# Kernel optimization log

Measured on AMD Instinct MI355X. Metric: run time of the kernel, lower is better.

The kernel has to match this reference:

```python
import jax, jax.numpy as jnp
import numpy as np

N_ANGLES = 180
N_DETECTORS = 256


def _bilinear_sample(img, x, y):
    """Bilinear sample img[y, x]; zero outside. img: [H, W]; x, y: any shape."""
    H, W = img.shape
    x0 = jnp.floor(x)
    y0 = jnp.floor(y)
    xi = x0.astype(jnp.int32)
    yi = y0.astype(jnp.int32)
    wx = x - x0
    wy = y - y0

    def get(ix, iy):
        valid = (ix >= 0) & (ix < W) & (iy >= 0) & (iy < H)
        ixc = jnp.clip(ix, 0, W - 1)
        iyc = jnp.clip(iy, 0, H - 1)
        return jnp.where(valid, img[iyc, ixc], jnp.zeros((), img.dtype))

    v00 = get(xi, yi)
    v01 = get(xi + 1, yi)
    v10 = get(xi, yi + 1)
    v11 = get(xi + 1, yi + 1)
    return (v00 * (1.0 - wx) + v01 * wx) * (1.0 - wy) + (v10 * (1.0 - wx) + v11 * wx) * wy


def setup_inputs() -> dict:
    key = jax.random.key(0)
    inputs = jax.random.uniform(key, (8, 256, 256, 1), dtype=jnp.float32)
    return {"inputs": inputs}


def reference(inputs):
    # Parallel-beam forward Radon transform (forwardproject).
    # inputs: [B, H, W, 1] image batch -> sinogram [B, n_angles, n_detectors, 1]
    B, H, W, _ = inputs.shape
    A, D = N_ANGLES, N_DETECTORS
    T = H  # integration samples along each ray

    theta = jnp.linspace(0.0, jnp.pi, A, endpoint=False, dtype=inputs.dtype)
    cos_t = jnp.cos(theta)[:, None, None]  # [A,1,1]
    sin_t = jnp.sin(theta)[:, None, None]

    s = (jnp.arange(D, dtype=inputs.dtype) - (D - 1) / 2.0)[None, :, None]  # detector offsets
    t = (jnp.arange(T, dtype=inputs.dtype) - (T - 1) / 2.0)[None, None, :]  # along-ray offsets

    cx = (W - 1) / 2.0
    cy = (H - 1) / 2.0
    # sample coords for every (angle, detector, ray-step): [A, D, T]
    x = cx + s * cos_t - t * sin_t
    y = cy + s * sin_t + t * cos_t

    imgs = inputs[..., 0]  # [B, H, W]
    vals = jax.vmap(lambda im: _bilinear_sample(im, x, y))(imgs)  # [B, A, D, T]
    sino = vals.sum(axis=-1)  # ray integral (unit step length)
    return sino[..., None]  # [B, A, D, 1]
```

## Files before the change

### kernel.cpp

```cpp
#include <hip/hip_runtime.h>
#include <math.h>

#define NA    180
#define HB    9
#define KB    29
#define PC    262
#define PR    263
#define TROWS 11
#define TSZ   (PC * TROWS)
#define OUTN  (8 * NA * 256)
#define APG   4
#define NG    23

typedef _Float16 h2  __attribute__((ext_vector_type(2)));
typedef _Float16 h8  __attribute__((ext_vector_type(8)));
typedef __fp16   hf2 __attribute__((ext_vector_type(2)));

__device__ __forceinline__ h2 pkrtz(float a, float b) {
    hf2 t = __builtin_amdgcn_cvt_pkrtz(a, b);
    return __builtin_bit_cast(h2, t);
}
__device__ __forceinline__ float fdot2f(h2 a, h2 b, float c) {
#if __has_builtin(__builtin_amdgcn_fdot2)
    return __builtin_amdgcn_fdot2(__builtin_bit_cast(hf2, a),
                                  __builtin_bit_cast(hf2, b), c, false);
#else
    return c + (float)a.x * (float)b.x + (float)a.y * (float)b.y;
#endif
}
__device__ __forceinline__ float imc(const float* im, int y, int x) {
    return ((unsigned)y < 256u && (unsigned)x < 256u) ? im[(y << 8) + x] : 0.0f;
}

__global__ __launch_bounds__(256) void prep_kernel(
    const float* __restrict__ img, uint4* __restrict__ P0,
    uint4* __restrict__ P1, float* __restrict__ out, float* __restrict__ tab)
{
    const int tid = threadIdx.x;
    const int row = blockIdx.x;
    const int mb  = blockIdx.y;

    if (mb == 0) {
        for (int i = row * 256 + tid; i < OUTN; i += PR * 256) out[i] = 0.0f;
    }
    if (mb == 1 && row == 0 && tid < NA) {
        const float theta = (float)tid * ((float)M_PI / (float)NA);
        tab[tid]      = cosf(theta);
        tab[tid + NA] = sinf(theta);
    }

    const int bg = mb & 1;
    const float* im0 = img + ((size_t)(bg * 4) << 16);
    const int v = row - 3;

    if (mb < 2) {
        uint4* dst = P0 + (size_t)(bg * PR + row) * PC;
        for (int j = tid; j < PC; j += 256) {
            const int u = j - 2;
            h8 t = {};
            if (j < 261) {
                t[0] = (_Float16)imc(im0,             v, u); t[1] = (_Float16)imc(im0,             v + 1, u);
                t[2] = (_Float16)imc(im0 + (1 << 16), v, u); t[3] = (_Float16)imc(im0 + (1 << 16), v + 1, u);
                t[4] = (_Float16)imc(im0 + (2 << 16), v, u); t[5] = (_Float16)imc(im0 + (2 << 16), v + 1, u);
                t[6] = (_Float16)imc(im0 + (3 << 16), v, u); t[7] = (_Float16)imc(im0 + (3 << 16), v + 1, u);
            }
            dst[j] = __builtin_bit_cast(uint4, t);
        }
    } else {
        uint4* dst = P1 + (size_t)(bg * PR + row) * PC;
        for (int j = tid; j < PC; j += 256) {
            const int u = j - 2;
            h8 t = {};
            if (j < 261) {
                t[0] = (_Float16)imc(im0,             u, v); t[1] = (_Float16)imc(im0,             u, v + 1);
                t[2] = (_Float16)imc(im0 + (1 << 16), u, v); t[3] = (_Float16)imc(im0 + (1 << 16), u, v + 1);
                t[4] = (_Float16)imc(im0 + (2 << 16), u, v); t[5] = (_Float16)imc(im0 + (2 << 16), u, v + 1);
                t[6] = (_Float16)imc(im0 + (3 << 16), u, v); t[7] = (_Float16)imc(im0 + (3 << 16), u, v + 1);
            }
            dst[j] = __builtin_bit_cast(uint4, t);
        }
    }
}

#define SAMPLE(JV, UV, VPV, A0, A1, A2, A3)                                   \
    {                                                                         \
        const float ucl = fminf(fmaxf((UV), -1.5f), 257.5f);                  \
        const float uf = floorf(ucl);                                         \
        const float wu = ucl - uf;                                            \
        const float vf = floorf(VPV);                                         \
        const float wv = (VPV) - vf;                                          \
        const float vfc = fminf(fmaxf(vf, -1.0f), 9.0f);                      \
        const int idx = (int)fmaf(vfc, (float)PC, uf) + (PC + 2);             \
        const h8 A8 = __builtin_bit_cast(h8, s_tile[idx]);                    \
        const h8 B8 = __builtin_bit_cast(h8, s_tile[idx + 1]);                \
        const h2 wu2 = pkrtz(wu, wu);                                         \
        const h8 wu8 = __builtin_shufflevector(wu2, wu2, 0,1,0,1,0,1,0,1);    \
        const h8 tb8 = (B8 - A8) * wu8 + A8;                                  \
        h2 wv2 = pkrtz(1.0f - wv, wv);                                        \
        wv2 = ((unsigned)(JV) < span) ? wv2 : hz;                             \
        A0 = fdot2f(__builtin_shufflevector(tb8, tb8, 0, 1), wv2, A0);        \
        A1 = fdot2f(__builtin_shufflevector(tb8, tb8, 2, 3), wv2, A1);        \
        A2 = fdot2f(__builtin_shufflevector(tb8, tb8, 4, 5), wv2, A2);        \
        A3 = fdot2f(__builtin_shufflevector(tb8, tb8, 6, 7), wv2, A3);        \
    }

template<bool MODEX>
__device__ __forceinline__ void radon_body(
    const uint4* __restrict__ Pbase,
    float* __restrict__ out, const float* __restrict__ tab,
    uint4* s_tile, int tid, int b0, int p, int gi)
{
    const int lo = -2 + p * HB;

    {
        const uint4* src = Pbase + (size_t)(lo + 2) * PC;
        for (int i = tid; i < TSZ; i += 256) s_tile[i] = src[i];
    }
    __syncthreads();

    const float detf = (float)tid - 127.5f;
    const float lof = (float)lo;
    const h2 hz = {};

    for (int g = 0; g < APG; ++g) {
        const int ai = gi * APG + g;
        int a;
        if (MODEX) { if (ai >= 89) break; a = 46 + ai; }
        else       { if (ai >= 91) break; a = (ai <= 45) ? ai : 89 + ai; }

        const float c = tab[a];
        const float s = tab[a + NA];

        const float xc = 127.5f + detf * c + 127.5f * s;
        const float yc = 127.5f + detf * s - 127.5f * c;

        const float ucst = MODEX ? yc : xc;
        const float vcst = MODEX ? xc : yc;
        const float du   = MODEX ? c  : -s;
        const float dv   = MODEX ? -s : c;

        const float inv = 1.0f / dv;
        const float f1 = (lof - vcst) * inv;
        const float f2 = (lof + (float)HB - vcst) * inv;
        const float fmn = fminf(f1, f2);
        const float fmx = fmaxf(f1, f2);
        int kmin, kend;
        if (dv > 0.0f) { kmin = (int)ceilf(fmn);      kend = (int)ceilf(fmx); }
        else           { kmin = (int)floorf(fmn) + 1; kend = (int)floorf(fmx) + 1; }

        const int len = kend - kmin;
        const int jlo = max(0, -kmin);
        const int jhi = min(len, 256 - kmin);
        const int spani = max(0, jhi - jlo);
        if (!__any(spani > 0)) continue;
        const unsigned span = (unsigned)spani;

        const int kstart = kmin + jlo;
        const int Lmax = (int)((float)HB * fabsf(inv)) + 2;

        float u  = fmaf((float)kstart, du, ucst);
        float vp = fmaf((float)kstart, dv, vcst - lof);
        const float du2 = du + du, dv2 = dv + dv;
        const float du3 = du2 + du, dv3 = dv2 + dv;
        const float du4 = du2 + du2, dv4 = dv2 + dv2;

        float a0 = 0.f, a1 = 0.f, a2 = 0.f, a3 = 0.f;
        float e0 = 0.f, e1 = 0.f, e2 = 0.f, e3 = 0.f;
        float c0 = 0.f, c1 = 0.f, c2 = 0.f, c3 = 0.f;
        float d0 = 0.f, d1 = 0.f, d2 = 0.f, d3 = 0.f;

        int j = 0;
        for (; j + 3 < Lmax; j += 4) {
            SAMPLE(j,     u,        vp,        a0, a1, a2, a3);
            SAMPLE(j + 1, u + du,   vp + dv,   e0, e1, e2, e3);
            SAMPLE(j + 2, u + du2,  vp + dv2,  c0, c1, c2, c3);
            SAMPLE(j + 3, u + du3,  vp + dv3,  d0, d1, d2, d3);
            u += du4; vp += dv4;
        }
        for (; j + 1 < Lmax; j += 2) {
            SAMPLE(j,     u,      vp,      a0, a1, a2, a3);
            SAMPLE(j + 1, u + du, vp + dv, e0, e1, e2, e3);
            u += du2; vp += dv2;
        }
        if (j < Lmax) SAMPLE(j, u, vp, a0, a1, a2, a3);

        if (spani > 0) {
            float* o = &out[((b0 * NA + a) << 8) + tid];
            atomicAdd(o,                 (a0 + c0) + (e0 + d0));
            atomicAdd(o + (NA << 8),     (a1 + c1) + (e1 + d1));
            atomicAdd(o + 2 * (NA << 8), (a2 + c2) + (e2 + d2));
            atomicAdd(o + 3 * (NA << 8), (a3 + c3) + (e3 + d3));
        }
    }
}

__global__ __launch_bounds__(256, 3) void radon_kernel(
    const uint4* __restrict__ P0, const uint4* __restrict__ P1,
    float* __restrict__ out, const float* __restrict__ tab)
{
    __shared__ uint4 s_tile[TSZ];
    const int tid = threadIdx.x;
    const int bg  = blockIdx.x;
    const int p   = blockIdx.y;
    const int gid = blockIdx.z;
    const int b0  = bg * 4;
    if (gid < NG)
        radon_body<false>(P0 + (size_t)bg * PR * PC, out, tab, s_tile, tid, b0, p, gid);
    else
        radon_body<true>(P1 + (size_t)bg * PR * PC, out, tab, s_tile, tid, b0, p, gid - NG);
}

extern "C" void kernel_launch(void* const* d_in, const int* in_sizes, int n_in,
                              void* d_out, int out_size, void* d_ws, size_t ws_size,
                              hipStream_t stream) {
    const float* img = (const float*)d_in[0];
    float* out = (float*)d_out;

    uint4* P0 = (uint4*)d_ws;
    uint4* P1 = P0 + (size_t)2 * PR * PC;
    float* tab = (float*)(P1 + (size_t)2 * PR * PC);

    prep_kernel<<<dim3(PR, 4), 256, 0, stream>>>(img, P0, P1, out, tab);
    radon_kernel<<<dim3(2, KB, 2 * NG), 256, 0, stream>>>(P0, P1, out, tab);
}
```

Before: 112.2 us.

## Pack all 8 batch images per texel and bilinear-sample in fp32 accumulators

The prep kernel now packs all 8 batch images into one 16-byte texel per pixel, where before it packed 4 images times 2 rows. Each sample therefore does 4 LDS reads and serves all 8 batches, and interpolation along v is done in fp16 with the u weight folded into fp32 FMAs instead of fdot2. Tiles are 8 rows tall, there are 2 angles per group, occupancy rises to 4 blocks, and the per-angle loop length becomes a wave-max span computed with shuffles instead of a fixed Lmax. The intent is to cut redundant index math and sample bookkeeping across batch groups. In exchange each sample issues more LDS loads and more FMAs per lane, and the accumulators use more registers.

New measurement: 108.5 us. -3.3%, faster.

```diff
diff --git a/kernel.cpp b/kernel.cpp
--- a/kernel.cpp
+++ b/kernel.cpp
@@ -2,15 +2,16 @@
 #include <math.h>
 
 #define NA    180
-#define HB    9
-#define KB    29
+#define HB    8
+#define KB    33
 #define PC    262
-#define PR    263
-#define TROWS 11
+#define PR    266
+#define TROWS 9
 #define TSZ   (PC * TROWS)
 #define OUTN  (8 * NA * 256)
-#define APG   4
-#define NG    23
+#define APG   2
+#define NGY   46
+#define NGX   45
 
 typedef _Float16 h2  __attribute__((ext_vector_type(2)));
 typedef _Float16 h8  __attribute__((ext_vector_type(8)));
@@ -19,14 +20,6 @@
 __device__ __forceinline__ h2 pkrtz(float a, float b) {
     hf2 t = __builtin_amdgcn_cvt_pkrtz(a, b);
     return __builtin_bit_cast(h2, t);
-}
-__device__ __forceinline__ float fdot2f(h2 a, h2 b, float c) {
-#if __has_builtin(__builtin_amdgcn_fdot2)
-    return __builtin_amdgcn_fdot2(__builtin_bit_cast(hf2, a),
-                                  __builtin_bit_cast(hf2, b), c, false);
-#else
-    return c + (float)a.x * (float)b.x + (float)a.y * (float)b.y;
-#endif
 }
 __device__ __forceinline__ float imc(const float* im, int y, int x) {
     return ((unsigned)y < 256u && (unsigned)x < 256u) ? im[(y << 8) + x] : 0.0f;
@@ -49,78 +42,80 @@
         tab[tid + NA] = sinf(theta);
     }
 
-    const int bg = mb & 1;
-    const float* im0 = img + ((size_t)(bg * 4) << 16);
     const int v = row - 3;
-
-    if (mb < 2) {
-        uint4* dst = P0 + (size_t)(bg * PR + row) * PC;
-        for (int j = tid; j < PC; j += 256) {
-            const int u = j - 2;
-            h8 t = {};
-            if (j < 261) {
-                t[0] = (_Float16)imc(im0,             v, u); t[1] = (_Float16)imc(im0,             v + 1, u);
-                t[2] = (_Float16)imc(im0 + (1 << 16), v, u); t[3] = (_Float16)imc(im0 + (1 << 16), v + 1, u);
-                t[4] = (_Float16)imc(im0 + (2 << 16), v, u); t[5] = (_Float16)imc(im0 + (2 << 16), v + 1, u);
-                t[6] = (_Float16)imc(im0 + (3 << 16), v, u); t[7] = (_Float16)imc(im0 + (3 << 16), v + 1, u);
+    uint4* dst = (mb == 0 ? P0 : P1) + (size_t)row * PC;
+    for (int j = tid; j < PC; j += 256) {
+        const int u = j - 2;
+        h8 t = {};
+        if (j < 261) {
+            if (mb == 0) {
+                #pragma unroll
+                for (int b = 0; b < 8; ++b)
+                    t[b] = (_Float16)imc(img + ((size_t)b << 16), v, u);
+            } else {
+                #pragma unroll
+                for (int b = 0; b < 8; ++b)
+                    t[b] = (_Float16)imc(img + ((size_t)b << 16), u, v);
             }
-            dst[j] = __builtin_bit_cast(uint4, t);
-        }
-    } else {
-        uint4* dst = P1 + (size_t)(bg * PR + row) * PC;
-        for (int j = tid; j < PC; j += 256) {
-            const int u = j - 2;
-            h8 t = {};
-            if (j < 261) {
-                t[0] = (_Float16)imc(im0,             u, v); t[1] = (_Float16)imc(im0,             u, v + 1);
-                t[2] = (_Float16)imc(im0 + (1 << 16), u, v); t[3] = (_Float16)imc(im0 + (1 << 16), u, v + 1);
-                t[4] = (_Float16)imc(im0 + (2 << 16), u, v); t[5] = (_Float16)imc(im0 + (2 << 16), u, v + 1);
-                t[6] = (_Float16)imc(im0 + (3 << 16), u, v); t[7] = (_Float16)imc(im0 + (3 << 16), u, v + 1);
-            }
-            dst[j] = __builtin_bit_cast(uint4, t);
-        }
-    }
-}
-
-#define SAMPLE(JV, UV, VPV, A0, A1, A2, A3)                                   \
+        }
+        dst[j] = __builtin_bit_cast(uint4, t);
+    }
+}
+
+#define SAMPLE8(JV, UV, VPV, ACC)                                             \
     {                                                                         \
         const float ucl = fminf(fmaxf((UV), -1.5f), 257.5f);                  \
         const float uf = floorf(ucl);                                         \
         const float wu = ucl - uf;                                            \
-        const float vf = floorf(VPV);                                         \
+        float vf = floorf(VPV);                                               \
+        vf = fminf(fmaxf(vf, 0.0f), 7.0f);                                    \
         const float wv = (VPV) - vf;                                          \
-        const float vfc = fminf(fmaxf(vf, -1.0f), 9.0f);                      \
-        const int idx = (int)fmaf(vfc, (float)PC, uf) + (PC + 2);             \
-        const h8 A8 = __builtin_bit_cast(h8, s_tile[idx]);                    \
-        const h8 B8 = __builtin_bit_cast(h8, s_tile[idx + 1]);                \
-        const h2 wu2 = pkrtz(wu, wu);                                         \
-        const h8 wu8 = __builtin_shufflevector(wu2, wu2, 0,1,0,1,0,1,0,1);    \
-        const h8 tb8 = (B8 - A8) * wu8 + A8;                                  \
-        h2 wv2 = pkrtz(1.0f - wv, wv);                                        \
-        wv2 = ((unsigned)(JV) < span) ? wv2 : hz;                             \
-        A0 = fdot2f(__builtin_shufflevector(tb8, tb8, 0, 1), wv2, A0);        \
-        A1 = fdot2f(__builtin_shufflevector(tb8, tb8, 2, 3), wv2, A1);        \
-        A2 = fdot2f(__builtin_shufflevector(tb8, tb8, 4, 5), wv2, A2);        \
-        A3 = fdot2f(__builtin_shufflevector(tb8, tb8, 6, 7), wv2, A3);        \
+        const int idx = (int)fmaf(vf, (float)PC, uf) + 2;                     \
+        const h8 ra0 = __builtin_bit_cast(h8, s_tile[idx]);                   \
+        const h8 ra1 = __builtin_bit_cast(h8, s_tile[idx + 1]);               \
+        const h8 rb0 = __builtin_bit_cast(h8, s_tile[idx + PC]);              \
+        const h8 rb1 = __builtin_bit_cast(h8, s_tile[idx + PC + 1]);          \
+        const h2 wv2 = pkrtz(wv, wv);                                         \
+        const h8 wv8 = __builtin_shufflevector(wv2, wv2, 0,1,0,1,0,1,0,1);    \
+        const h8 v0 = (rb0 - ra0) * wv8 + ra0;                                \
+        const h8 v1 = (rb1 - ra1) * wv8 + ra1;                                \
+        const float ws = ((unsigned)(JV) < span) ? 1.0f : 0.0f;               \
+        const float fw1 = ws * wu;                                            \
+        const float fw0 = ws - fw1;                                           \
+        ACC[0] = fmaf((float)v0[0], fw0, ACC[0]);                             \
+        ACC[0] = fmaf((float)v1[0], fw1, ACC[0]);                             \
+        ACC[1] = fmaf((float)v0[1], fw0, ACC[1]);                             \
+        ACC[1] = fmaf((float)v1[1], fw1, ACC[1]);                             \
+        ACC[2] = fmaf((float)v0[2], fw0, ACC[2]);                             \
+        ACC[2] = fmaf((float)v1[2], fw1, ACC[2]);                             \
+        ACC[3] = fmaf((float)v0[3], fw0, ACC[3]);                             \
+        ACC[3] = fmaf((float)v1[3], fw1, ACC[3]);                             \
+        ACC[4] = fmaf((float)v0[4], fw0, ACC[4]);                             \
+        ACC[4] = fmaf((float)v1[4], fw1, ACC[4]);                             \
+        ACC[5] = fmaf((float)v0[5], fw0, ACC[5]);                             \
+        ACC[5] = fmaf((float)v1[5], fw1, ACC[5]);                             \
+        ACC[6] = fmaf((float)v0[6], fw0, ACC[6]);                             \
+        ACC[6] = fmaf((float)v1[6], fw1, ACC[6]);                             \
+        ACC[7] = fmaf((float)v0[7], fw0, ACC[7]);                             \
+        ACC[7] = fmaf((float)v1[7], fw1, ACC[7]);                             \
     }
 
 template<bool MODEX>
 __device__ __forceinline__ void radon_body(
     const uint4* __restrict__ Pbase,
     float* __restrict__ out, const float* __restrict__ tab,
-    uint4* s_tile, int tid, int b0, int p, int gi)
+    uint4* s_tile, int tid, int p, int gi)
 {
     const int lo = -2 + p * HB;
 
     {
-        const uint4* src = Pbase + (size_t)(lo + 2) * PC;
+        const uint4* src = Pbase + (size_t)(lo + 3) * PC;
         for (int i = tid; i < TSZ; i += 256) s_tile[i] = src[i];
     }
     __syncthreads();
 
     const float detf = (float)tid - 127.5f;
     const float lof = (float)lo;
-    const h2 hz = {};
 
     for (int g = 0; g < APG; ++g) {
         const int ai = gi * APG + g;
@@ -139,9 +134,11 @@
         const float du   = MODEX ? c  : -s;
         const float dv   = MODEX ? -s : c;
 
+        const float vlo_f = fmaxf(lof, -1.0f);
+        const float vhi_f = fminf(lof + (float)HB, 256.0f);
         const float inv = 1.0f / dv;
-        const float f1 = (lof - vcst) * inv;
-        const float f2 = (lof + (float)HB - vcst) * inv;
+        const float f1 = (vlo_f - vcst) * inv;
+        const float f2 = (vhi_f - vcst) * inv;
         const float fmn = fminf(f1, f2);
         const float fmx = fmaxf(f1, f2);
         int kmin, kend;
@@ -152,11 +149,19 @@
         const int jlo = max(0, -kmin);
         const int jhi = min(len, 256 - kmin);
         const int spani = max(0, jhi - jlo);
-        if (!__any(spani > 0)) continue;
+
+        int m = spani;
+        m = max(m, __shfl_xor(m, 1));
+        m = max(m, __shfl_xor(m, 2));
+        m = max(m, __shfl_xor(m, 4));
+        m = max(m, __shfl_xor(m, 8));
+        m = max(m, __shfl_xor(m, 16));
+        m = max(m, __shfl_xor(m, 32));
+        const int mspan = __builtin_amdgcn_readfirstlane(m);
+        if (mspan <= 0) continue;
         const unsigned span = (unsigned)spani;
 
         const int kstart = kmin + jlo;
-        const int Lmax = (int)((float)HB * fabsf(inv)) + 2;
 
         float u  = fmaf((float)kstart, du, ucst);
         float vp = fmaf((float)kstart, dv, vcst - lof);
@@ -164,50 +169,45 @@
         const float du3 = du2 + du, dv3 = dv2 + dv;
         const float du4 = du2 + du2, dv4 = dv2 + dv2;
 
-        float a0 = 0.f, a1 = 0.f, a2 = 0.f, a3 = 0.f;
-        float e0 = 0.f, e1 = 0.f, e2 = 0.f, e3 = 0.f;
-        float c0 = 0.f, c1 = 0.f, c2 = 0.f, c3 = 0.f;
-        float d0 = 0.f, d1 = 0.f, d2 = 0.f, d3 = 0.f;
+        float accA[8] = {}, accB[8] = {}, accC[8] = {}, accD[8] = {};
 
         int j = 0;
-        for (; j + 3 < Lmax; j += 4) {
-            SAMPLE(j,     u,        vp,        a0, a1, a2, a3);
-            SAMPLE(j + 1, u + du,   vp + dv,   e0, e1, e2, e3);
-            SAMPLE(j + 2, u + du2,  vp + dv2,  c0, c1, c2, c3);
-            SAMPLE(j + 3, u + du3,  vp + dv3,  d0, d1, d2, d3);
+        for (; j + 3 < mspan; j += 4) {
+            SAMPLE8(j,     u,       vp,       accA);
+            SAMPLE8(j + 1, u + du,  vp + dv,  accB);
+            SAMPLE8(j + 2, u + du2, vp + dv2, accC);
+            SAMPLE8(j + 3, u + du3, vp + dv3, accD);
             u += du4; vp += dv4;
         }
-        for (; j + 1 < Lmax; j += 2) {
-            SAMPLE(j,     u,      vp,      a0, a1, a2, a3);
-            SAMPLE(j + 1, u + du, vp + dv, e0, e1, e2, e3);
+        for (; j + 1 < mspan; j += 2) {
+            SAMPLE8(j,     u,      vp,      accA);
+            SAMPLE8(j + 1, u + du, vp + dv, accB);
             u += du2; vp += dv2;
         }
-        if (j < Lmax) SAMPLE(j, u, vp, a0, a1, a2, a3);
+        if (j < mspan) SAMPLE8(j, u, vp, accA);
 
         if (spani > 0) {
-            float* o = &out[((b0 * NA + a) << 8) + tid];
-            atomicAdd(o,                 (a0 + c0) + (e0 + d0));
-            atomicAdd(o + (NA << 8),     (a1 + c1) + (e1 + d1));
-            atomicAdd(o + 2 * (NA << 8), (a2 + c2) + (e2 + d2));
-            atomicAdd(o + 3 * (NA << 8), (a3 + c3) + (e3 + d3));
-        }
-    }
-}
-
-__global__ __launch_bounds__(256, 3) void radon_kernel(
+            float* o = &out[(a << 8) + tid];
+            #pragma unroll
+            for (int b = 0; b < 8; ++b)
+                atomicAdd(o + b * (NA << 8),
+                          (accA[b] + accC[b]) + (accB[b] + accD[b]));
+        }
+    }
+}
+
+__global__ __launch_bounds__(256, 4) void radon_kernel(
     const uint4* __restrict__ P0, const uint4* __restrict__ P1,
     float* __restrict__ out, const float* __restrict__ tab)
 {
     __shared__ uint4 s_tile[TSZ];
     const int tid = threadIdx.x;
-    const int bg  = blockIdx.x;
-    const int p   = blockIdx.y;
-    const int gid = blockIdx.z;
-    const int b0  = bg * 4;
-    if (gid < NG)
-        radon_body<false>(P0 + (size_t)bg * PR * PC, out, tab, s_tile, tid, b0, p, gid);
+    const int p   = blockIdx.x;
+    const int gid = blockIdx.y;
+    if (gid < NGY)
+        radon_body<false>(P0, out, tab, s_tile, tid, p, gid);
     else
-        radon_body<true>(P1 + (size_t)bg * PR * PC, out, tab, s_tile, tid, b0, p, gid - NG);
+        radon_body<true >(P1, out, tab, s_tile, tid, p, gid - NGY);
 }
 
 extern "C" void kernel_launch(void* const* d_in, const int* in_sizes, int n_in,
@@ -217,9 +217,9 @@
     float* out = (float*)d_out;
 
     uint4* P0 = (uint4*)d_ws;
-    uint4* P1 = P0 + (size_t)2 * PR * PC;
-    float* tab = (float*)(P1 + (size_t)2 * PR * PC);
-
-    prep_kernel<<<dim3(PR, 4), 256, 0, stream>>>(img, P0, P1, out, tab);
-    radon_kernel<<<dim3(2, KB, 2 * NG), 256, 0, stream>>>(P0, P1, out, tab);
-}
+    uint4* P1 = P0 + (size_t)PR * PC;
+    float* tab = (float*)(P1 + (size_t)PR * PC);
+
+    prep_kernel<<<dim3(PR, 2), 256, 0, stream>>>(img, P0, P1, out, tab);
+    radon_kernel<<<dim3(KB, NGY + NGX), 256, 0, stream>>>(P0, P1, out, tab);
+}
```
